# Kernel tuning notes

Hardware: AMD Instinct MI355X
Metric: run time of the kernel (lower is better)

Reference implementation:

```python
import jax, jax.numpy as jnp
import numpy as np

SUB, E_NO, I_NO = 20, 2000, 500
T_DATA, T_SYN, T_HIST = 20000, 200, 50
SB, HB = 3, 3


def setup_inputs() -> dict:
    key = jax.random.key(0)
    ks = jax.random.split(key, 14)
    S_e = (jax.random.uniform(ks[0], (T_DATA, E_NO)) < 0.02).astype(jnp.float32)
    S_i = (jax.random.uniform(ks[1], (T_DATA, I_NO)) < 0.02).astype(jnp.float32)
    C_den = (jax.random.uniform(ks[2], (SUB, SUB)) < 0.1).astype(jnp.float32)
    C_syn_e = (jax.random.uniform(ks[3], (SUB, E_NO)) < 0.05).astype(jnp.float32)
    C_syn_i = (jax.random.uniform(ks[4], (SUB, I_NO)) < 0.05).astype(jnp.float32)
    W_syn = 0.1 * jax.random.normal(ks[5], (SUB, SB, 2))
    Tau_syn = jnp.tile(jnp.arange(SB, dtype=jnp.float32)[:, None], (1, 2))
    Delta_syn = jax.random.uniform(ks[6], (SUB, 2))
    W_hist = 0.1 * jax.random.normal(ks[7], (SUB, HB))
    Tau_hist = jnp.arange(HB, dtype=jnp.float32)
    Delta_hist = jax.random.uniform(ks[8], (SUB,))
    W_sub = jax.random.uniform(ks[9], (SUB,))
    V_o = jax.random.normal(ks[10], (1,))
    Theta = jnp.zeros((SUB,), jnp.float32)
    return {"S_e": S_e, "S_i": S_i, "C_den": C_den, "C_syn_e": C_syn_e,
            "C_syn_i": C_syn_i, "W_syn": W_syn, "Tau_syn": Tau_syn,
            "Delta_syn": Delta_syn, "W_hist": W_hist, "Tau_hist": Tau_hist,
            "Delta_hist": Delta_hist, "W_sub": W_sub, "V_o": V_o, "Theta": Theta}


def _alpha_kernels(delta, tau_log, W, T):
    # delta: [sub], tau_log: [B], W: [sub, B] -> kernels [sub, T]
    t = jnp.maximum(jnp.arange(T, dtype=jnp.float32)[None, :] - delta[:, None], 0.0)  # [sub,T]
    tt = t[:, None, :] / jnp.exp(tau_log)[None, :, None]  # [sub,B,T]
    return jnp.einsum('sbt,sb->st', tt * jnp.exp(-tt), W)


def _causal_conv(x, kern):
    # x: [T, sub], kern: [sub, T_k]; out[t,s] = sum_k kern[s,k] * x[t-k,s]
    Tk = kern.shape[1]
    xp = jnp.pad(x.T[None], ((0, 0), (0, 0), (Tk - 1, 0)))  # [1, sub, T+Tk-1]
    out = jax.lax.conv_general_dilated(
        xp, jnp.flip(kern, 1)[:, None, :], (1,), 'VALID',
        feature_group_count=kern.shape[0])
    return out[0].T  # [T, sub]


def reference(S_e, S_i, C_den, C_syn_e, C_syn_i, W_syn, Tau_syn, Delta_syn,
              W_hist, Tau_hist, Delta_hist, W_sub, V_o, Theta):
    # --- synaptic drive (vectorized over subunits) ---
    ke = _alpha_kernels(jnp.exp(Delta_syn[:, 0]), Tau_syn[:, 0], W_syn[:, :, 0], T_SYN)
    ki = _alpha_kernels(jnp.exp(Delta_syn[:, 1]), Tau_syn[:, 1], W_syn[:, :, 1], T_SYN)
    in_e = S_e @ C_syn_e.T  # [T, sub]
    in_i = S_i @ C_syn_i.T
    syn_in = _causal_conv(in_e, ke) + _causal_conv(in_i, ki)  # [T, sub]

    # --- history kernel ---
    hist_kern = _alpha_kernels(Delta_hist, Tau_hist, W_hist, T_HIST)  # [sub, T_hist]
    K = jnp.flip(hist_kern, 1)  # K[s, j] multiplies buffer entry j (oldest first)

    # --- sequential recurrence via scan ---
    def step(buf, syn_t):
        # buf: [T_hist, sub] = Y_pad[t : t+T_hist]
        h = jnp.einsum('js,sj->s', buf, K)
        prop = (buf[-1] * W_sub) @ C_den.T
        y = jnp.tanh(syn_t + prop + Theta + h)
        buf = jnp.concatenate([buf[1:], y[None]], 0)
        return buf, y

    buf0 = jnp.zeros((T_HIST, SUB), syn_in.dtype)
    _, Y = jax.lax.scan(step, buf0, syn_in)  # Y: [T, sub]
    return Y[:, 0] * W_sub[0] + V_o[0]
```

## Files before the change

kernel.cpp:

```cpp
#include <hip/hip_runtime.h>
#include <hip/hip_bf16.h>
#include <stdint.h>

#define SUBU 20
#define E_NO 2000
#define I_NO 500
#define T_DATA 20000
#define T_SYNK 200
#define T_HISTK 50
#define SBAS 3
#define HBAS 3
#define TPAD 20096
#define KSTORE 12

#define OFF_SYN  0
#define OFF_INE  401920
#define OFF_INI  803840
#define OFF_KE   1205760
#define OFF_KI   1209760
#define OFF_IIR  1213760
#define OFF_MW   1214760
#define OFF_MIDX 1215000
#define OFF_PAR  1215240
#define OFF_FLAG 1215264
#define OFF_Y    OFF_INI

#define TKC 2.8853900817779268f

__device__ __forceinline__ float bf2f(unsigned short u){
  unsigned v = ((unsigned)u) << 16; float f; __builtin_memcpy(&f, &v, 4); return f;
}
__device__ __forceinline__ float ldany(const void* p, int i, int bf){
  return bf ? bf2f(((const unsigned short*)p)[i]) : ((const float*)p)[i];
}

__global__ __launch_bounds__(256) void k_detect(const void* s_e, int* flag){
  __shared__ int found;
  if (threadIdx.x == 0) found = 0;
  __syncthreads();
  const unsigned* w = (const unsigned*)s_e;
  int hit = 0;
  for (int i = threadIdx.x; i < 8192; i += 256){
    unsigned x = w[i];
    if (x == 0x00003F80u || x == 0x3F803F80u) hit = 1;
  }
  if (hit) atomicOr(&found, 1);
  __syncthreads();
  if (threadIdx.x == 0) *flag = found;
}

__global__ __launch_bounds__(512) void k_prep(
    const void* Cden, const void* Wsyn, const void* Tausyn, const void* Dsyn,
    const void* Whist, const void* Tauhist, const void* Dhist,
    const void* Wsub, const void* Vo, const void* Theta, float* ws){
  int* wsi = (int*)ws;
  const int bf = wsi[OFF_FLAG];
  const int tx = threadIdx.x;
  __shared__ int mx;
  if (tx == 0) mx = 0;
  __syncthreads();
  for (int idx = tx; idx < SUBU * T_SYNK; idx += 512){
    int s = idx / T_SYNK, t = idx % T_SYNK;
    for (int c = 0; c < 2; ++c){
      float delta = __expf(ldany(Dsyn, s*2 + c, bf));
      float acc = 0.f;
      for (int b = 0; b < SBAS; ++b){
        float tau = __expf(ldany(Tausyn, b*2 + c, bf));
        float w   = ldany(Wsyn, (s*SBAS + b)*2 + c, bf);
        float tt  = fmaxf((float)t - delta, 0.f) / tau;
        acc += w * tt * __expf(-tt);
      }
      ws[(c == 0 ? OFF_KE : OFF_KI) + s*T_SYNK + t] = acc;
    }
  }
  if (tx < SUBU * HBAS){
    int s = tx / HBAS, b = tx % HBAS;
    float tau = __expf(ldany(Tauhist, b, bf));
    float w   = TKC * ldany(Whist, s*HBAS + b, bf);
    float dl  = ldany(Dhist, s, bf);
    float rho = __expf(-1.f / tau);
    float e1  = __expf(-(1.f - dl) / tau);
    float g1  = ((1.f - dl) / tau) * e1;
    float kap = rho / tau;
    float* c = ws + OFF_IIR + s*16 + b*4;
    c[0] = rho;
    c[1] = w * kap;
    c[2] = w * g1;
    c[3] = e1;
    if (b == 2){
      float e49 = __expf(-(49.f - dl) / tau);
      float g49 = ((49.f - dl) / tau) * e49;
      ws[OFF_IIR + s*16 + 12] = w * (rho*g49 + kap*e49);
      ws[OFF_IIR + s*16 + 13] = rho * e49;
    }
  }
  if (tx < SUBU){
    int s = tx, cnt = 0;
    float rowsum = 0.f;
    for (int sp = 0; sp < SUBU; ++sp){
      float c = ldany(Cden, s*SUBU + sp, bf);
      if (c != 0.f && cnt < KSTORE){
        float m = c * ldany(Wsub, sp, bf);
        rowsum += m;
        ws[OFF_MW + s*KSTORE + cnt]  = -2.f * TKC * m;
        wsi[OFF_MIDX + s*KSTORE + cnt] = sp;
        ++cnt;
      }
    }
    for (int k = cnt; k < KSTORE; ++k){
      ws[OFF_MW + s*KSTORE + k] = 0.f; wsi[OFF_MIDX + s*KSTORE + k] = 0;
    }
    atomicMax(&mx, cnt);
    ws[OFF_PAR + s] = TKC * (ldany(Theta, s, bf) + rowsum);
  }
  __syncthreads();
  if (tx == 0){
    ws[OFF_PAR + SUBU]     = ldany(Wsub, 0, bf);
    ws[OFF_PAR + SUBU + 1] = ldany(Vo, 0, bf);
    wsi[OFF_PAR + 23] = (mx <= 6) ? 6 : 12;
  }
}

template<int BF>
__device__ __forceinline__ void gemm_impl(const void* S, const void* C, int W,
                                          float* dst, int t0, int lane){
  float acc[4][SUBU];
  #pragma unroll
  for (int r = 0; r < 4; ++r)
    #pragma unroll
    for (int s = 0; s < SUBU; ++s) acc[r][s] = 0.f;
  for (int e = lane; e < W; e += 64){
    float s0 = ldany(S, (t0+0)*W + e, BF);
    float s1 = ldany(S, (t0+1)*W + e, BF);
    float s2 = ldany(S, (t0+2)*W + e, BF);
    float s3 = ldany(S, (t0+3)*W + e, BF);
    #pragma unroll
    for (int s = 0; s < SUBU; ++s){
      float c = ldany(C, s*W + e, BF);
      acc[0][s] = fmaf(s0, c, acc[0][s]);
      acc[1][s] = fmaf(s1, c, acc[1][s]);
      acc[2][s] = fmaf(s2, c, acc[2][s]);
      acc[3][s] = fmaf(s3, c, acc[3][s]);
    }
  }
  #pragma unroll
  for (int r = 0; r < 4; ++r){
    #pragma unroll
    for (int s = 0; s < SUBU; ++s){
      float v = acc[r][s];
      #pragma unroll
      for (int m = 32; m >= 1; m >>= 1) v += __shfl_xor(v, m, 64);
      if (lane == 0) dst[s*TPAD + t0 + r] = v;
    }
  }
}

__global__ __launch_bounds__(64) void k_gemm(const void* S, const void* C, int W,
                                             float* dst, const int* flagp){
  int t0 = blockIdx.x * 4, lane = threadIdx.x;
  if (*flagp) gemm_impl<1>(S, C, W, dst, t0, lane);
  else        gemm_impl<0>(S, C, W, dst, t0, lane);
}

__global__ __launch_bounds__(256) void k_conv(float* ws){
  const int s  = blockIdx.y;
  const int t0 = blockIdx.x * 256;
  const float* ine = ws + OFF_INE + s*TPAD;
  const float* ini = ws + OFF_INI + s*TPAD;
  __shared__ float eL[455], iL[455], keL[T_SYNK], kiL[T_SYNK];
  for (int j = threadIdx.x; j < 455; j += 256){
    int t = t0 - 199 + j;
    bool ok = (t >= 0 && t < TPAD);
    eL[j] = ok ? ine[t] : 0.f;
    iL[j] = ok ? ini[t] : 0.f;
  }
  for (int j = threadIdx.x; j < T_SYNK; j += 256){
    keL[j] = ws[OFF_KE + s*T_SYNK + j];
    kiL[j] = ws[OFF_KI + s*T_SYNK + j];
  }
  __syncthreads();
  int t = t0 + threadIdx.x;
  if (t < TPAD){
    float a0 = 0.f, a1 = 0.f;
    #pragma unroll 4
    for (int k = 0; k < T_SYNK; ++k){
      a0 = fmaf(keL[k], eL[threadIdx.x + 199 - k], a0);
      a1 = fmaf(kiL[k], iL[threadIdx.x + 199 - k], a1);
    }
    ws[OFF_SYN + s*TPAD + t] = fmaf(TKC, a0 + a1, ws[OFF_PAR + s]);
  }
}

__device__ __forceinline__ float get4(const float4& a, const float4& b,
                                      const float4& c, const float4& d, int u){
  const float4& q = (u < 4) ? a : ((u < 8) ? b : ((u < 12) ? c : d));
  int r = u & 3;
  return (r == 0) ? q.x : ((r == 1) ? q.y : ((r == 2) ? q.z : q.w));
}
__device__ __forceinline__ void set4(float4& a, float4& b, float4& c, float4& d,
                                     int u, float v){
  float4& q = (u < 4) ? a : ((u < 8) ? b : ((u < 12) ? c : d));
  int r = u & 3;
  if (r == 0) q.x = v; else if (r == 1) q.y = v; else if (r == 2) q.z = v; else q.w = v;
}

template<int KM, int BF>
__global__ __launch_bounds__(64, 1) void k_scan(float* ws, float* yout){
  const int* wsi = (const int*)ws;
  if ((wsi[OFF_FLAG] != 0) != (BF != 0)) return;
  if (wsi[OFF_PAR + 23] != KM) return;
  const int lane = threadIdx.x;
  const int s = lane < SUBU ? lane : SUBU - 1;
  float mwp[KM]; int mad[KM];
  #pragma unroll
  for (int k = 0; k < KM; ++k){
    mwp[k] = ws[OFF_MW + s*KSTORE + k];
    mad[k] = wsi[OFF_MIDX + s*KSTORE + k] * 4;
  }
  const float* cc = ws + OFF_IIR + s*16;
  const float rh0 = cc[0],  kp0 = cc[1],  ay0 = cc[2],  ey0 = cc[3];
  const float rh1 = cc[4],  kp1 = cc[5],  ay1 = cc[6],  ey1 = cc[7];
  const float rh2 = cc[8],  kp2 = cc[9],  ay2 = cc[10], ey2 = cc[11];
  const float cA  = cc[12], cE  = cc[13];
  const float wsub0 = ws[OFF_PAR + SUBU];
  const float vo    = ws[OFF_PAR + SUBU + 1];
  const float* syncol = ws + OFF_SYN + s*TPAD;

  float yhv[66];
  #pragma unroll
  for (int j = 0; j < 66; ++j) yhv[j] = 0.f;
  float A0 = 0.f, E0 = 0.f, A1 = 0.f, E1 = 0.f, A2 = 0.f, E2 = 0.f;
  float pb[KM];
  #pragma unroll
  for (int k = 0; k < KM; ++k) pb[k] = 0.5f;
  float4 u0 = *(const float4*)(syncol + 0);
  float4 u1 = *(const float4*)(syncol + 4);
  float4 u2 = *(const float4*)(syncol + 8);
  float4 u3 = *(const float4*)(syncol + 12);
  float4 n0, n1, n2, n3;
  float xpre = u0.x;

  auto block16 = [&](int tbase, float4& b0, float4& b1, float4& b2, float4& b3,
                     float4& p0, float4& p1, float4& p2, float4& p3){
    const float4* src = (const float4*)(syncol + tbase + 16);
    p0 = src[0]; p1 = src[1]; p2 = src[2]; p3 = src[3];
    float4 ob0, ob1, ob2, ob3;
    #pragma unroll
    for (int u = 0; u < 16; ++u){
      float acc0 = fmaf(mwp[0], pb[0], xpre);
      float acc1 = mwp[1] * pb[1];
      #pragma unroll
      for (int k = 2; k + 1 < KM; k += 2){
        acc0 = fmaf(mwp[k],   pb[k],   acc0);
        acc1 = fmaf(mwp[k+1], pb[k+1], acc1);
      }
      float X  = acc0 + acc1;
      float ex = __builtin_amdgcn_exp2f(X);
      float r  = __builtin_amdgcn_rcpf(ex + 1.f);
      int rb = __float_as_int(r);
      #pragma unroll
      for (int k = 0; k < KM; ++k)
        pb[k] = __int_as_float(__builtin_amdgcn_ds_bpermute(mad[k], rb));
      float y = fmaf(-2.f, r, 1.f);
      float yprev = yhv[u + 49];
      float yold  = yhv[u];
      float A0n = fmaf(rh0, A0, fmaf(kp0, E0, ay0 * yprev));
      E0 = fmaf(rh0, E0, ey0 * yprev); A0 = A0n;
      float A1n = fmaf(rh1, A1, fmaf(kp1, E1, ay1 * yprev));
      E1 = fmaf(rh1, E1, ey1 * yprev); A1 = A1n;
      float A2n = fmaf(rh2, A2, fmaf(kp2, E2, fmaf(-cA, yold, ay2 * yprev)));
      E2 = fmaf(rh2, E2, fmaf(-cE, yold, ey2 * yprev)); A2 = A2n;
      float h = (A0 + A1) + A2;
      float cn = (u < 15) ? get4(b0, b1, b2, b3, u + 1) : p0.x;
      xpre = cn + h;
      yhv[u + 50] = y;
      set4(ob0, ob1, ob2, ob3, u, fmaf(y, wsub0, vo));
    }
    #pragma unroll
    for (int j = 0; j < 50; ++j) yhv[j] = yhv[j + 16];
    if (lane == 0 && tbase + 16 <= T_DATA){
      float4* q = (float4*)(yout + tbase);
      q[0] = ob0; q[1] = ob1; q[2] = ob2; q[3] = ob3;
    }
  };

  #pragma unroll 1
  for (int ib = 0; ib < 628; ++ib){
    block16(ib*32,      u0, u1, u2, u3, n0, n1, n2, n3);
    block16(ib*32 + 16, n0, n1, n2, n3, u0, u1, u2, u3);
  }
}

__global__ __launch_bounds__(256) void k_out(const float* ws, void* outp){
  const int* wsi = (const int*)ws;
  if (wsi[OFF_FLAG] == 0) return;
  int i = blockIdx.x * 256 + threadIdx.x;
  if (i < T_DATA)
    ((__hip_bfloat16*)outp)[i] = __float2bfloat16(ws[OFF_Y + i]);
}

extern "C" void kernel_launch(void* const* d_in, const int* in_sizes, int n_in,
                              void* d_out, int out_size, void* d_ws, size_t ws_size,
                              hipStream_t stream){
  const void* S_e   = d_in[0];
  const void* S_i   = d_in[1];
  const void* C_den = d_in[2];
  const void* C_e   = d_in[3];
  const void* C_i   = d_in[4];
  const void* W_syn = d_in[5];
  const void* Tau_s = d_in[6];
  const void* D_syn = d_in[7];
  const void* W_hst = d_in[8];
  const void* Tau_h = d_in[9];
  const void* D_hst = d_in[10];
  const void* W_sub = d_in[11];
  const void* V_o   = d_in[12];
  const void* Theta = d_in[13];
  float* ws = (float*)d_ws;
  int* flagp = (int*)(ws + OFF_FLAG);

  k_detect<<<1, 256, 0, stream>>>(S_e, flagp);
  k_prep<<<1, 512, 0, stream>>>(C_den, W_syn, Tau_s, D_syn, W_hst, Tau_h, D_hst,
                                W_sub, V_o, Theta, ws);
  k_gemm<<<5000, 64, 0, stream>>>(S_e, C_e, E_NO, ws + OFF_INE, flagp);
  k_gemm<<<5000, 64, 0, stream>>>(S_i, C_i, I_NO, ws + OFF_INI, flagp);
  dim3 cgrid(79, 20);
  k_conv<<<cgrid, 256, 0, stream>>>(ws);
  k_scan<6, 0><<<1, 64, 0, stream>>>(ws, (float*)d_out);
  k_scan<6, 1><<<1, 64, 0, stream>>>(ws, ws + OFF_Y);
  k_scan<12, 0><<<1, 64, 0, stream>>>(ws, (float*)d_out);
  k_scan<12, 1><<<1, 64, 0, stream>>>(ws, ws + OFF_Y);
  k_out<<<79, 256, 0, stream>>>(ws, d_out);
}
```

Measured before the change: 2.160 ms.

## Specialize scan on smaller neighbor counts, store r history, merge detect into prep

The scan kernel now keeps the sigmoid reciprocal r in its history instead of y, with coefficients rescaled so tanh's affine transform folds into the IIR updates. The history shift happens once per 32 steps using compile-time offsets rather than after every 16-step block. New template variants for 3 and 4 dendritic neighbours shorten the per-step dot product when connectivity is sparse. The detect kernel is merged into prep, and the GEMM uses 256-thread blocks. The scan always writes to the workspace, and the output kernel converts for both dtypes, adding one copy pass.

```diff
diff --git a/kernel.cpp b/kernel.cpp
--- a/kernel.cpp
+++ b/kernel.cpp
@@ -1,17 +1,16 @@
 #include <hip/hip_runtime.h>
 #include <hip/hip_bf16.h>
 #include <stdint.h>
+#include <type_traits>
 
 #define SUBU 20
 #define E_NO 2000
 #define I_NO 500
 #define T_DATA 20000
 #define T_SYNK 200
-#define T_HISTK 50
+#define HBAS 3
 #define SBAS 3
-#define HBAS 3
 #define TPAD 20096
-#define KSTORE 12
 
 #define OFF_SYN  0
 #define OFF_INE  401920
@@ -24,6 +23,7 @@
 #define OFF_PAR  1215240
 #define OFF_FLAG 1215264
 #define OFF_Y    OFF_INI
+#define KSTORE   12
 
 #define TKC 2.8853900817779268f
 
@@ -33,32 +33,30 @@
 __device__ __forceinline__ float ldany(const void* p, int i, int bf){
   return bf ? bf2f(((const unsigned short*)p)[i]) : ((const float*)p)[i];
 }
-
-__global__ __launch_bounds__(256) void k_detect(const void* s_e, int* flag){
-  __shared__ int found;
-  if (threadIdx.x == 0) found = 0;
-  __syncthreads();
-  const unsigned* w = (const unsigned*)s_e;
-  int hit = 0;
-  for (int i = threadIdx.x; i < 8192; i += 256){
-    unsigned x = w[i];
-    if (x == 0x00003F80u || x == 0x3F803F80u) hit = 1;
-  }
-  if (hit) atomicOr(&found, 1);
-  __syncthreads();
-  if (threadIdx.x == 0) *flag = found;
-}
+__device__ __forceinline__ float ex2(float x){ return __builtin_amdgcn_exp2f(x); }
+__device__ __forceinline__ float rcpa(float x){ return __builtin_amdgcn_rcpf(x); }
 
 __global__ __launch_bounds__(512) void k_prep(
-    const void* Cden, const void* Wsyn, const void* Tausyn, const void* Dsyn,
-    const void* Whist, const void* Tauhist, const void* Dhist,
+    const void* Se, const void* Cden, const void* Wsyn, const void* Tausyn,
+    const void* Dsyn, const void* Whist, const void* Tauhist, const void* Dhist,
     const void* Wsub, const void* Vo, const void* Theta, float* ws){
   int* wsi = (int*)ws;
-  const int bf = wsi[OFF_FLAG];
   const int tx = threadIdx.x;
-  __shared__ int mx;
-  if (tx == 0) mx = 0;
+  __shared__ int found, mx;
+  if (tx == 0){ found = 0; mx = 0; }
   __syncthreads();
+  {
+    const unsigned* w = (const unsigned*)Se;
+    int hit = 0;
+    for (int i = tx; i < 8192; i += 512){
+      unsigned x = w[i];
+      if (x == 0x00003F80u || x == 0x3F803F80u) hit = 1;
+    }
+    if (hit) atomicOr(&found, 1);
+  }
+  __syncthreads();
+  const int bf = found;
+  if (tx == 0) wsi[OFF_FLAG] = bf;
   for (int idx = tx; idx < SUBU * T_SYNK; idx += 512){
     int s = idx / T_SYNK, t = idx % T_SYNK;
     for (int c = 0; c < 2; ++c){
@@ -117,7 +115,7 @@
   if (tx == 0){
     ws[OFF_PAR + SUBU]     = ldany(Wsub, 0, bf);
     ws[OFF_PAR + SUBU + 1] = ldany(Vo, 0, bf);
-    wsi[OFF_PAR + 23] = (mx <= 6) ? 6 : 12;
+    wsi[OFF_PAR + 23] = (mx <= 3) ? 3 : (mx <= 4 ? 4 : (mx <= 6 ? 6 : 12));
   }
 }
 
@@ -155,9 +153,10 @@
   }
 }
 
-__global__ __launch_bounds__(64) void k_gemm(const void* S, const void* C, int W,
-                                             float* dst, const int* flagp){
-  int t0 = blockIdx.x * 4, lane = threadIdx.x;
+__global__ __launch_bounds__(256) void k_gemm(const void* S, const void* C, int W,
+                                              float* dst, const int* flagp){
+  const int wave = threadIdx.x >> 6, lane = threadIdx.x & 63;
+  const int t0 = blockIdx.x * 16 + wave * 4;
   if (*flagp) gemm_impl<1>(S, C, W, dst, t0, lane);
   else        gemm_impl<0>(S, C, W, dst, t0, lane);
 }
@@ -204,10 +203,9 @@
   if (r == 0) q.x = v; else if (r == 1) q.y = v; else if (r == 2) q.z = v; else q.w = v;
 }
 
-template<int KM, int BF>
+template<int KM>
 __global__ __launch_bounds__(64, 1) void k_scan(float* ws, float* yout){
   const int* wsi = (const int*)ws;
-  if ((wsi[OFF_FLAG] != 0) != (BF != 0)) return;
   if (wsi[OFF_PAR + 23] != KM) return;
   const int lane = threadIdx.x;
   const int s = lane < SUBU ? lane : SUBU - 1;
@@ -218,18 +216,25 @@
     mad[k] = wsi[OFF_MIDX + s*KSTORE + k] * 4;
   }
   const float* cc = ws + OFF_IIR + s*16;
-  const float rh0 = cc[0],  kp0 = cc[1],  ay0 = cc[2],  ey0 = cc[3];
-  const float rh1 = cc[4],  kp1 = cc[5],  ay1 = cc[6],  ey1 = cc[7];
-  const float rh2 = cc[8],  kp2 = cc[9],  ay2 = cc[10], ey2 = cc[11];
-  const float cA  = cc[12], cE  = cc[13];
+  const float rh0 = cc[0], kp0 = cc[1], ayc0 = cc[2], eyc0 = cc[3];
+  const float rh1 = cc[4], kp1 = cc[5], ayc1 = cc[6], eyc1 = cc[7];
+  const float rh2 = cc[8], kp2 = cc[9];
+  const float cA = cc[12], cE = cc[13];
+  const float ayr0 = -2.f*ayc0, eyr0 = -2.f*eyc0;
+  const float ayr1 = -2.f*ayc1, eyr1 = -2.f*eyc1;
+  const float ayr2 = -2.f*cc[10], eyr2 = -2.f*cc[11];
+  const float cAr = 2.f*cA, cEr = 2.f*cE;
+  const float c2A = cc[10] - cA;
+  const float c2E = cc[11] - cE;
   const float wsub0 = ws[OFF_PAR + SUBU];
   const float vo    = ws[OFF_PAR + SUBU + 1];
+  const float m2w = -2.f * wsub0, wvo = wsub0 + vo;
   const float* syncol = ws + OFF_SYN + s*TPAD;
 
-  float yhv[66];
-  #pragma unroll
-  for (int j = 0; j < 66; ++j) yhv[j] = 0.f;
-  float A0 = 0.f, E0 = 0.f, A1 = 0.f, E1 = 0.f, A2 = 0.f, E2 = 0.f;
+  float rhv[82];
+  #pragma unroll
+  for (int j = 0; j < 82; ++j) rhv[j] = 0.5f;
+  float A0=0.f,E0=0.f,A1=0.f,E1=0.f,A2=0.f,E2=0.f;
   float pb[KM];
   #pragma unroll
   for (int k = 0; k < KM; ++k) pb[k] = 0.5f;
@@ -240,8 +245,9 @@
   float4 n0, n1, n2, n3;
   float xpre = u0.x;
 
-  auto block16 = [&](int tbase, float4& b0, float4& b1, float4& b2, float4& b3,
-                     float4& p0, float4& p1, float4& p2, float4& p3){
+  auto block16 = [&](auto OFS_, int tbase, float4& b0, float4& b1, float4& b2,
+                     float4& b3, float4& p0, float4& p1, float4& p2, float4& p3){
+    constexpr int OFS = decltype(OFS_)::value;
     const float4* src = (const float4*)(syncol + tbase + 16);
     p0 = src[0]; p1 = src[1]; p2 = src[2]; p3 = src[3];
     float4 ob0, ob1, ob2, ob3;
@@ -250,53 +256,56 @@
       float acc0 = fmaf(mwp[0], pb[0], xpre);
       float acc1 = mwp[1] * pb[1];
       #pragma unroll
-      for (int k = 2; k + 1 < KM; k += 2){
-        acc0 = fmaf(mwp[k],   pb[k],   acc0);
-        acc1 = fmaf(mwp[k+1], pb[k+1], acc1);
+      for (int k = 2; k < KM; ++k){
+        if (k & 1) acc1 = fmaf(mwp[k], pb[k], acc1);
+        else       acc0 = fmaf(mwp[k], pb[k], acc0);
       }
       float X  = acc0 + acc1;
-      float ex = __builtin_amdgcn_exp2f(X);
-      float r  = __builtin_amdgcn_rcpf(ex + 1.f);
+      float r  = rcpa(ex2(X) + 1.f);
       int rb = __float_as_int(r);
       #pragma unroll
       for (int k = 0; k < KM; ++k)
         pb[k] = __int_as_float(__builtin_amdgcn_ds_bpermute(mad[k], rb));
-      float y = fmaf(-2.f, r, 1.f);
-      float yprev = yhv[u + 49];
-      float yold  = yhv[u];
-      float A0n = fmaf(rh0, A0, fmaf(kp0, E0, ay0 * yprev));
-      E0 = fmaf(rh0, E0, ey0 * yprev); A0 = A0n;
-      float A1n = fmaf(rh1, A1, fmaf(kp1, E1, ay1 * yprev));
-      E1 = fmaf(rh1, E1, ey1 * yprev); A1 = A1n;
-      float A2n = fmaf(rh2, A2, fmaf(kp2, E2, fmaf(-cA, yold, ay2 * yprev)));
-      E2 = fmaf(rh2, E2, fmaf(-cE, yold, ey2 * yprev)); A2 = A2n;
+      float rp = rhv[OFS + u + 49];
+      float ro = rhv[OFS + u];
+      float A0n = fmaf(rh0, A0, fmaf(kp0, E0, fmaf(ayr0, rp, ayc0)));
+      E0 = fmaf(rh0, E0, fmaf(eyr0, rp, eyc0)); A0 = A0n;
+      float A1n = fmaf(rh1, A1, fmaf(kp1, E1, fmaf(ayr1, rp, ayc1)));
+      E1 = fmaf(rh1, E1, fmaf(eyr1, rp, eyc1)); A1 = A1n;
+      float A2n = fmaf(rh2, A2, fmaf(kp2, E2, fmaf(ayr2, rp, fmaf(cAr, ro, c2A))));
+      E2 = fmaf(rh2, E2, fmaf(eyr2, rp, fmaf(cEr, ro, c2E))); A2 = A2n;
       float h = (A0 + A1) + A2;
       float cn = (u < 15) ? get4(b0, b1, b2, b3, u + 1) : p0.x;
       xpre = cn + h;
-      yhv[u + 50] = y;
-      set4(ob0, ob1, ob2, ob3, u, fmaf(y, wsub0, vo));
-    }
-    #pragma unroll
-    for (int j = 0; j < 50; ++j) yhv[j] = yhv[j + 16];
+      rhv[OFS + u + 50] = r;
+      set4(ob0, ob1, ob2, ob3, u, fmaf(r, m2w, wvo));
+    }
     if (lane == 0 && tbase + 16 <= T_DATA){
       float4* q = (float4*)(yout + tbase);
       q[0] = ob0; q[1] = ob1; q[2] = ob2; q[3] = ob3;
     }
   };
 
+  using IC0  = std::integral_constant<int,0>;
+  using IC16 = std::integral_constant<int,16>;
   #pragma unroll 1
   for (int ib = 0; ib < 628; ++ib){
-    block16(ib*32,      u0, u1, u2, u3, n0, n1, n2, n3);
-    block16(ib*32 + 16, n0, n1, n2, n3, u0, u1, u2, u3);
+    block16(IC0{},  ib*32,      u0, u1, u2, u3, n0, n1, n2, n3);
+    block16(IC16{}, ib*32 + 16, n0, n1, n2, n3, u0, u1, u2, u3);
+    #pragma unroll
+    for (int j = 0; j < 50; ++j) rhv[j] = rhv[j + 32];
   }
 }
 
 __global__ __launch_bounds__(256) void k_out(const float* ws, void* outp){
   const int* wsi = (const int*)ws;
-  if (wsi[OFF_FLAG] == 0) return;
+  const int bf = wsi[OFF_FLAG];
   int i = blockIdx.x * 256 + threadIdx.x;
-  if (i < T_DATA)
-    ((__hip_bfloat16*)outp)[i] = __float2bfloat16(ws[OFF_Y + i]);
+  if (i < T_DATA){
+    float v = ws[OFF_Y + i];
+    if (bf) ((__hip_bfloat16*)outp)[i] = __float2bfloat16(v);
+    else    ((float*)outp)[i] = v;
+  }
 }
 
 extern "C" void kernel_launch(void* const* d_in, const int* in_sizes, int n_in,
@@ -319,16 +328,16 @@
   float* ws = (float*)d_ws;
   int* flagp = (int*)(ws + OFF_FLAG);
 
-  k_detect<<<1, 256, 0, stream>>>(S_e, flagp);
-  k_prep<<<1, 512, 0, stream>>>(C_den, W_syn, Tau_s, D_syn, W_hst, Tau_h, D_hst,
-                                W_sub, V_o, Theta, ws);
-  k_gemm<<<5000, 64, 0, stream>>>(S_e, C_e, E_NO, ws + OFF_INE, flagp);
-  k_gemm<<<5000, 64, 0, stream>>>(S_i, C_i, I_NO, ws + OFF_INI, flagp);
+  k_prep<<<1, 512, 0, stream>>>(S_e, C_den, W_syn, Tau_s, D_syn, W_hst, Tau_h,
+                                D_hst, W_sub, V_o, Theta, ws);
+  k_gemm<<<1250, 256, 0, stream>>>(S_e, C_e, E_NO, ws + OFF_INE, flagp);
+  k_gemm<<<1250, 256, 0, stream>>>(S_i, C_i, I_NO, ws + OFF_INI, flagp);
   dim3 cgrid(79, 20);
   k_conv<<<cgrid, 256, 0, stream>>>(ws);
-  k_scan<6, 0><<<1, 64, 0, stream>>>(ws, (float*)d_out);
-  k_scan<6, 1><<<1, 64, 0, stream>>>(ws, ws + OFF_Y);
-  k_scan<12, 0><<<1, 64, 0, stream>>>(ws, (float*)d_out);
-  k_scan<12, 1><<<1, 64, 0, stream>>>(ws, ws + OFF_Y);
+  float* yout = ws + OFF_Y;
+  k_scan<3><<<1, 64, 0, stream>>>(ws, yout);
+  k_scan<4><<<1, 64, 0, stream>>>(ws, yout);
+  k_scan<6><<<1, 64, 0, stream>>>(ws, yout);
+  k_scan<12><<<1, 64, 0, stream>>>(ws, yout);
   k_out<<<79, 256, 0, stream>>>(ws, d_out);
 }
```

After: 2.125 ms. No clear change (-1.6%).
